# Optimization experiments

Hardware: AMD Instinct MI355X
Metric: run time of the kernel (lower is better)

Reference implementation:

```python
import jax, jax.numpy as jnp
import numpy as np

B, S, D, H, MLP = 2, 2048, 1024, 16, 4096
DH = D // H
EPS_LN = 1e-6
KERNEL_EPS = 1e-3  # fast_attention generalized kernel_epsilon


def layer_norm(x, scale, bias):
    m = jnp.mean(x, axis=-1, keepdims=True)
    v = jnp.mean(jnp.square(x - m), axis=-1, keepdims=True)
    return (x - m) * jax.lax.rsqrt(v + EPS_LN) * scale + bias


def performer_causal_attention(q, k, v):
    """FAVOR+ generalized attention (deterministic relu features), causal.

    q,k,v: [B,S,H,DH]. phi(x) = relu(x) + eps. Linear-time via prefix sums:
      out_i = phi(q_i) . cumsum_j<=i phi(k_j) v_j^T / (phi(q_i) . cumsum phi(k_j))
    """
    phi_q = jax.nn.relu(q) + KERNEL_EPS          # [B,S,H,M]
    phi_k = jax.nn.relu(k) + KERNEL_EPS          # [B,S,H,M]
    kv = jnp.cumsum(jnp.einsum('bshm,bshd->bshmd', phi_k, v), axis=1)  # [B,S,H,M,DH]
    num = jnp.einsum('bshm,bshmd->bshd', phi_q, kv)
    den = jnp.einsum('bshm,bshm->bsh', phi_q, jnp.cumsum(phi_k, axis=1))
    return num / den[..., None]


def setup_inputs() -> dict:
    key = jax.random.key(0)
    ks = jax.random.split(key, 7)
    def w(k, shape, scale):
        return jax.random.normal(k, shape, jnp.float32) * scale
    s_in = 1.0 / np.sqrt(D)
    return {
        'inputs': jax.random.normal(ks[0], (B, S, D), jnp.float32),
        'ln1_scale': jnp.ones((D,), jnp.float32),
        'ln1_bias': jnp.zeros((D,), jnp.float32),
        'wq': w(ks[1], (D, H, DH), s_in),
        'wk': w(ks[2], (D, H, DH), s_in),
        'wv': w(ks[3], (D, H, DH), s_in),
        'wo': w(ks[4], (H, DH, D), s_in),
        'ln2_scale': jnp.ones((D,), jnp.float32),
        'ln2_bias': jnp.zeros((D,), jnp.float32),
        'w1': w(ks[5], (D, MLP), s_in),
        'b1': jnp.zeros((MLP,), jnp.float32),
        'w2': w(ks[6], (MLP, D), 1.0 / np.sqrt(MLP)),
        'b2': jnp.zeros((D,), jnp.float32),
    }


def reference(inputs, ln1_scale, ln1_bias, wq, wk, wv, wo,
              ln2_scale, ln2_bias, w1, b1, w2, b2):
    # pre-LN self-attention (Performer FAVOR+ generalized, causal)
    x = layer_norm(inputs, ln1_scale, ln1_bias)
    q = jnp.einsum('bsd,dhm->bshm', x, wq)
    k = jnp.einsum('bsd,dhm->bshm', x, wk)
    v = jnp.einsum('bsd,dhm->bshm', x, wv)
    attn = performer_causal_attention(q, k, v)          # [B,S,H,DH]
    attn_out = jnp.einsum('bshm,hmd->bsd', attn, wo)    # output projection
    x = attn_out + inputs                               # residual
    # pre-LN MLP block
    y = layer_norm(x, ln2_scale, ln2_bias)
    y = jax.nn.gelu(y @ w1 + b1) @ w2 + b2
    return x + y
```

## Files before the change

### kernel.cpp

```cpp
#include <hip/hip_runtime.h>
#include <math.h>
#include <stdint.h>

typedef __bf16 bf16;
typedef bf16  bf16x8 __attribute__((ext_vector_type(8)));
typedef float f32x4  __attribute__((ext_vector_type(4)));

constexpr int Bb  = 2;
constexpr int Ss  = 2048;
constexpr int Dd  = 1024;
constexpr int Hh  = 16;
constexpr int DHh = 64;
constexpr int MLPd = 4096;
constexpr int ROWS = Bb * Ss;
constexpr int NC  = Ss / 64;
constexpr int BH  = Bb * Hh;
constexpr float EPS_LN = 1e-6f;
constexpr float KEPS   = 1e-3f;

__device__ __forceinline__ void async_copy16(const bf16* g, bf16* l) {
    __builtin_amdgcn_global_load_lds(
        (__attribute__((address_space(1))) void*)g,
        (__attribute__((address_space(3))) void*)l,
        16, 0, 0);
}

__device__ __forceinline__ int swz64(int row, int col) {
    return row * 64 + (((col >> 3) ^ row) & 7) * 8 + (col & 7);
}

__global__ __launch_bounds__(256) void ln_kernel(const float* __restrict__ x,
                                                 const float* __restrict__ scale,
                                                 const float* __restrict__ bias,
                                                 bf16* __restrict__ out)
{
    const int row = blockIdx.x;
    const float* xr = x + (size_t)row * Dd;
    float vals[4];
    float sum = 0.f, sumsq = 0.f;
#pragma unroll
    for (int i = 0; i < 4; i++) {
        float v = xr[threadIdx.x + 256 * i];
        vals[i] = v;
        sum += v;
        sumsq += v * v;
    }
#pragma unroll
    for (int off = 32; off > 0; off >>= 1) {
        sum   += __shfl_down(sum, off);
        sumsq += __shfl_down(sumsq, off);
    }
    __shared__ float ssum[4], ssq[4];
    const int wave = threadIdx.x >> 6;
    if ((threadIdx.x & 63) == 0) { ssum[wave] = sum; ssq[wave] = sumsq; }
    __syncthreads();
    const float tot   = ssum[0] + ssum[1] + ssum[2] + ssum[3];
    const float totsq = ssq[0] + ssq[1] + ssq[2] + ssq[3];
    const float mean = tot * (1.f / Dd);
    const float var  = totsq * (1.f / Dd) - mean * mean;
    const float r = rsqrtf(var + EPS_LN);
    bf16* orow = out + (size_t)row * Dd;
#pragma unroll
    for (int i = 0; i < 4; i++) {
        const int c = threadIdx.x + 256 * i;
        orow[c] = (bf16)((vals[i] - mean) * r * scale[c] + bias[c]);
    }
}

__global__ __launch_bounds__(256) void convert_T(const float* __restrict__ in,
                                                 bf16* __restrict__ out,
                                                 int K, int N)
{
    __shared__ float tile[32][33];
    const int k0 = blockIdx.y * 32, n0 = blockIdx.x * 32;
    const int tx = threadIdx.x & 31, ty = threadIdx.x >> 5;
#pragma unroll
    for (int i = 0; i < 32; i += 8)
        tile[ty + i][tx] = in[(size_t)(k0 + ty + i) * N + n0 + tx];
    __syncthreads();
#pragma unroll
    for (int i = 0; i < 32; i += 8)
        out[(size_t)(n0 + ty + i) * K + k0 + tx] = (bf16)tile[tx][ty + i];
}

__global__ __launch_bounds__(256) void convert_T4(const float* __restrict__ s0,
                                                  const float* __restrict__ s1,
                                                  const float* __restrict__ s2,
                                                  const float* __restrict__ s3,
                                                  bf16* __restrict__ d0,
                                                  bf16* __restrict__ d1,
                                                  bf16* __restrict__ d2,
                                                  bf16* __restrict__ d3)
{
    const float* in  = (blockIdx.z == 0) ? s0 : (blockIdx.z == 1) ? s1
                     : (blockIdx.z == 2) ? s2 : s3;
    bf16* out        = (blockIdx.z == 0) ? d0 : (blockIdx.z == 1) ? d1
                     : (blockIdx.z == 2) ? d2 : d3;
    __shared__ float tile[32][33];
    const int k0 = blockIdx.y * 32, n0 = blockIdx.x * 32;
    const int tx = threadIdx.x & 31, ty = threadIdx.x >> 5;
#pragma unroll
    for (int i = 0; i < 32; i += 8)
        tile[ty + i][tx] = in[(size_t)(k0 + ty + i) * 1024 + n0 + tx];
    __syncthreads();
#pragma unroll
    for (int i = 0; i < 32; i += 8)
        out[(size_t)(n0 + ty + i) * 1024 + k0 + tx] = (bf16)tile[tx][ty + i];
}

enum { EP_QKV = 0, EP_NONE = 1, EP_RES = 2, EP_GELU = 3, EP_BIAS_RES = 4 };

template <int TN, int BK, int NDIM, int KDIM, int MODE>
__global__ __launch_bounds__(256) void mfma_gemm(const bf16* __restrict__ A,
                                                 const bf16* __restrict__ BT,
                                                 void* __restrict__ Cout,
                                                 const float* __restrict__ bias,
                                                 const float* __restrict__ res,
                                                 bf16* __restrict__ out2,
                                                 bf16* __restrict__ out3)
{
    constexpr int WCT = TN / 2;
    constexpr int NJ  = TN / 32;
    constexpr int NS  = BK / 32;
    constexpr int CPR = BK / 8;
    constexpr int RPI = 2048 / BK;
    __shared__ bf16 As[128 * BK];
    __shared__ bf16 Bs[TN * BK];
    const int t = threadIdx.x;
    const int wave = t >> 6, lane = t & 63;
    const int row0 = blockIdx.y * 128, col0 = blockIdx.x * TN;
    const int wr = wave >> 1, wc = wave & 1;

    const int srow = t / CPR;
    const int gch  = (t % CPR) ^ (srow & 7);
    const int sdst = t * 8;

    const bf16* gA = A  + (size_t)(row0 + srow) * KDIM + gch * 8;
    const bf16* gB = BT + (size_t)(col0 + srow) * KDIM + gch * 8;

    const int m = lane & 15, quad = lane >> 4;
    const int mx7 = m & 7;

    f32x4 acc[4][NJ] = {};

    for (int k0 = 0; k0 < KDIM; k0 += BK) {
        __syncthreads();
#pragma unroll
        for (int i = 0; i < 128 / RPI; i++)
            async_copy16(gA + (size_t)i * RPI * KDIM, &As[i * 2048 + sdst]);
#pragma unroll
        for (int i = 0; i < TN / RPI; i++)
            async_copy16(gB + (size_t)i * RPI * KDIM, &Bs[i * 2048 + sdst]);
        __syncthreads();

#pragma unroll
        for (int s = 0; s < NS; s++) {
            const int pco = ((s * 4 + quad) ^ mx7) * 8;
            bf16x8 aF[4], bF[NJ];
#pragma unroll
            for (int i = 0; i < 4; i++)
                aF[i] = *(const bf16x8*)&As[(wr * 64 + i * 16 + m) * BK + pco];
#pragma unroll
            for (int j = 0; j < NJ; j++)
                bF[j] = *(const bf16x8*)&Bs[(wc * WCT + j * 16 + m) * BK + pco];
#pragma unroll
            for (int i = 0; i < 4; i++)
#pragma unroll
                for (int j = 0; j < NJ; j++)
                    acc[i][j] = __builtin_amdgcn_mfma_f32_16x16x32_bf16(
                        aF[i], bF[j], acc[i][j], 0, 0, 0);
        }
        gA += BK;
        gB += BK;
    }

    bf16* qkv_dst = nullptr;
    int col_base = col0;
    bool do_phi = false;
    if constexpr (MODE == EP_QKV) {
        const int third = col0 >> 10;
        qkv_dst = (third == 0) ? (bf16*)Cout : (third == 1) ? out2 : out3;
        col_base = col0 & 1023;
        do_phi = (third < 2);
    }

#pragma unroll
    for (int i = 0; i < 4; i++) {
#pragma unroll
        for (int j = 0; j < NJ; j++) {
#pragma unroll
            for (int r = 0; r < 4; r++) {
                const int row = row0 + wr * 64 + i * 16 + quad * 4 + r;
                const int col = col0 + wc * WCT + j * 16 + m;
                float val = acc[i][j][r];
                if constexpr (MODE == EP_QKV) {
                    const int lc = col_base + wc * WCT + j * 16 + m;
                    if (do_phi) val = fmaxf(val, 0.f) + KEPS;
                    qkv_dst[(size_t)row * 1024 + lc] = (bf16)val;
                } else if constexpr (MODE == EP_NONE) {
                    ((bf16*)Cout)[(size_t)row * NDIM + col] = (bf16)val;
                } else if constexpr (MODE == EP_RES) {
                    ((float*)Cout)[(size_t)row * NDIM + col] = val + res[(size_t)row * NDIM + col];
                } else if constexpr (MODE == EP_GELU) {
                    val += bias[col];
                    const float u = 0.7978845608028654f * (val + 0.044715f * val * val * val);
                    const float e = __expf(2.f * u);
                    val = val * (1.f - 1.f / (e + 1.f));
                    ((bf16*)Cout)[(size_t)row * NDIM + col] = (bf16)val;
                } else {
                    val += bias[col] + res[(size_t)row * NDIM + col];
                    ((float*)Cout)[(size_t)row * NDIM + col] = val;
                }
            }
        }
    }
}

__global__ __launch_bounds__(256) void chunk_kv_kernel(const bf16* __restrict__ phik,
                                                       const bf16* __restrict__ v,
                                                       bf16* __restrict__ kvs,
                                                       float* __restrict__ ksums)
{
    const int c = blockIdx.x, bh = blockIdx.y;
    const int b = bh >> 4, h = bh & 15;
    __shared__ bf16 Kt[64 * 64];
    __shared__ bf16 Vt[64 * 64];
    const int t = threadIdx.x;
    const int wave = t >> 6, lane = t & 63;
    const int m16 = lane & 15, quad = lane >> 4;
    const int wr = wave >> 1, wc = wave & 1;
    const int f = t & 63, s4 = t >> 6;

#pragma unroll
    for (int i = 0; i < 16; i++) {
        const int s = s4 + 4 * i;
        const size_t g = ((size_t)((b * Ss + c * 64 + s) * Hh + h)) * DHh + f;
        Kt[swz64(f, s)] = phik[g];
        Vt[swz64(f, s)] = v[g];
    }
    __syncthreads();

    f32x4 acc[2][2] = {};
#pragma unroll
    for (int ks = 0; ks < 2; ks++) {
        bf16x8 aF[2], bF[2];
#pragma unroll
        for (int i = 0; i < 2; i++)
            aF[i] = *(const bf16x8*)&Kt[swz64(wr * 32 + i * 16 + m16, ks * 32 + quad * 8)];
#pragma unroll
        for (int j = 0; j < 2; j++)
            bF[j] = *(const bf16x8*)&Vt[swz64(wc * 32 + j * 16 + m16, ks * 32 + quad * 8)];
#pragma unroll
        for (int i = 0; i < 2; i++)
#pragma unroll
            for (int j = 0; j < 2; j++)
                acc[i][j] = __builtin_amdgcn_mfma_f32_16x16x32_bf16(
                    aF[i], bF[j], acc[i][j], 0, 0, 0);
    }

    const size_t base = ((size_t)bh * NC + c) * 4096;
#pragma unroll
    for (int i = 0; i < 2; i++)
#pragma unroll
        for (int j = 0; j < 2; j++)
#pragma unroll
            for (int r = 0; r < 4; r++) {
                const int mrow = wr * 32 + i * 16 + quad * 4 + r;
                const int dcol = wc * 32 + j * 16 + m16;
                kvs[base + mrow * 64 + dcol] = (bf16)acc[i][j][r];
            }

    if (t < 64) {
        float s_ = 0.f;
#pragma unroll
        for (int p = 0; p < 8; p++) {
            bf16x8 k8 = *(const bf16x8*)&Kt[t * 64 + p * 8];
#pragma unroll
            for (int e = 0; e < 8; e++) s_ += (float)k8[e];
        }
        ksums[((size_t)bh * NC + c) * 64 + t] = s_;
    }
}

__global__ __launch_bounds__(256) void scan_kernel(bf16* __restrict__ kvs,
                                                   float* __restrict__ ksums)
{
    const int e  = blockIdx.x * 256 + threadIdx.x;
    const int bh = blockIdx.y;
    float run = 0.f;
#pragma unroll 4
    for (int c = 0; c < NC; c++) {
        const size_t idx = ((size_t)bh * NC + c) * 4096 + e;
        const float val = (float)kvs[idx];
        kvs[idx] = (bf16)run;
        run += val;
    }
    if (blockIdx.x == 0 && threadIdx.x < 64) {
        float r = 0.f;
        for (int c = 0; c < NC; c++) {
            const size_t idx = ((size_t)bh * NC + c) * 64 + threadIdx.x;
            const float val = ksums[idx];
            ksums[idx] = r;
            r += val;
        }
    }
}

__global__ __launch_bounds__(256) void attn_out_kernel(const bf16* __restrict__ phiq,
                                                       const bf16* __restrict__ phik,
                                                       const bf16* __restrict__ v,
                                                       const bf16* __restrict__ kvs,
                                                       const float* __restrict__ ksums,
                                                       bf16* __restrict__ attn)
{
    const int c = blockIdx.x, bh = blockIdx.y;
    const int b = bh >> 4, h = bh & 15;
    __shared__ bf16 Qs [64 * 64];
    __shared__ bf16 KVb[64 * 64];
    __shared__ bf16 Sm [64 * 64];
    __shared__ bf16 KVt[64 * 64];
    __shared__ float ksm[64], den[64];
    const int t = threadIdx.x;
    const int wave = t >> 6, lane = t & 63;
    const int m16 = lane & 15, quad = lane >> 4;
    const int wr = wave >> 1, wc = wave & 1;
    const int f = t & 63, s4 = t >> 6;

#pragma unroll
    for (int i = 0; i < 16; i++) {
        const int s = s4 + 4 * i;
        const size_t g = ((size_t)((b * Ss + c * 64 + s) * Hh + h)) * DHh + f;
        Qs [swz64(s, f)] = phiq[g];
        KVb[swz64(s, f)] = phik[g];
    }
    if (t < 64) ksm[t] = ksums[((size_t)bh * NC + c) * 64 + t];
    __syncthreads();

    f32x4 sacc[2][2] = {};
#pragma unroll
    for (int ks = 0; ks < 2; ks++) {
        bf16x8 aF[2], bF[2];
#pragma unroll
        for (int i = 0; i < 2; i++)
            aF[i] = *(const bf16x8*)&Qs [swz64(wr * 32 + i * 16 + m16, ks * 32 + quad * 8)];
#pragma unroll
        for (int j = 0; j < 2; j++)
            bF[j] = *(const bf16x8*)&KVb[swz64(wc * 32 + j * 16 + m16, ks * 32 + quad * 8)];
#pragma unroll
        for (int i = 0; i < 2; i++)
#pragma unroll
            for (int j = 0; j < 2; j++)
                sacc[i][j] = __builtin_amdgcn_mfma_f32_16x16x32_bf16(
                    aF[i], bF[j], sacc[i][j], 0, 0, 0);
    }
#pragma unroll
    for (int i = 0; i < 2; i++)
#pragma unroll
        for (int j = 0; j < 2; j++)
#pragma unroll
            for (int r = 0; r < 4; r++) {
                const int row = wr * 32 + i * 16 + quad * 4 + r;
                const int col = wc * 32 + j * 16 + m16;
                Sm[swz64(row, col)] = (bf16)((col <= row) ? sacc[i][j][r] : 0.f);
            }
    __syncthreads();

#pragma unroll
    for (int i = 0; i < 16; i++) {
        const int s = s4 + 4 * i;
        const size_t g = ((size_t)((b * Ss + c * 64 + s) * Hh + h)) * DHh + f;
        KVb[swz64(f, s)] = v[g];
    }
    {
        const size_t base = ((size_t)bh * NC + c) * 4096;
#pragma unroll
        for (int i = 0; i < 16; i++) {
            const int e = t + 256 * i;
            KVt[swz64(e & 63, e >> 6)] = kvs[base + e];
        }
    }
    __syncthreads();

    if (t < 64) {
        float d_ = 0.f;
#pragma unroll
        for (int p = 0; p < 8; p++) {
            const int gc = (p ^ (t & 7)) * 8;
            bf16x8 q8 = *(const bf16x8*)&Qs[t * 64 + p * 8];
            bf16x8 s8 = *(const bf16x8*)&Sm[t * 64 + p * 8];
#pragma unroll
            for (int e = 0; e < 8; e++)
                d_ += (float)q8[e] * ksm[gc + e] + (float)s8[e];
        }
        den[t] = d_;
    }

    f32x4 oacc[2][2] = {};
#pragma unroll
    for (int ks = 0; ks < 2; ks++) {
        bf16x8 aF[2], bF[2];
#pragma unroll
        for (int i = 0; i < 2; i++)
            aF[i] = *(const bf16x8*)&Sm [swz64(wr * 32 + i * 16 + m16, ks * 32 + quad * 8)];
#pragma unroll
        for (int j = 0; j < 2; j++)
            bF[j] = *(const bf16x8*)&KVb[swz64(wc * 32 + j * 16 + m16, ks * 32 + quad * 8)];
#pragma unroll
        for (int i = 0; i < 2; i++)
#pragma unroll
            for (int j = 0; j < 2; j++)
                oacc[i][j] = __builtin_amdgcn_mfma_f32_16x16x32_bf16(
                    aF[i], bF[j], oacc[i][j], 0, 0, 0);
    }
#pragma unroll
    for (int ks = 0; ks < 2; ks++) {
        bf16x8 aF[2], bF[2];
#pragma unroll
        for (int i = 0; i < 2; i++)
            aF[i] = *(const bf16x8*)&Qs [swz64(wr * 32 + i * 16 + m16, ks * 32 + quad * 8)];
#pragma unroll
        for (int j = 0; j < 2; j++)
            bF[j] = *(const bf16x8*)&KVt[swz64(wc * 32 + j * 16 + m16, ks * 32 + quad * 8)];
#pragma unroll
        for (int i = 0; i < 2; i++)
#pragma unroll
            for (int j = 0; j < 2; j++)
                oacc[i][j] = __builtin_amdgcn_mfma_f32_16x16x32_bf16(
                    aF[i], bF[j], oacc[i][j], 0, 0, 0);
    }
    __syncthreads();

#pragma unroll
    for (int i = 0; i < 2; i++) {
#pragma unroll
        for (int r = 0; r < 4; r++) {
            const int row = wr * 32 + i * 16 + quad * 4 + r;
            const float dinv = 1.f / den[row];
#pragma unroll
            for (int j = 0; j < 2; j++) {
                const int col = wc * 32 + j * 16 + m16;
                attn[((size_t)((b * Ss + c * 64 + row) * Hh + h)) * DHh + col] =
                    (bf16)(oacc[i][j][r] * dinv);
            }
        }
    }
}

extern "C" void kernel_launch(void* const* d_in, const int* in_sizes, int n_in,
                              void* d_out, int out_size, void* d_ws, size_t ws_size,
                              hipStream_t stream)
{
    const float* inputs    = (const float*)d_in[0];
    const float* ln1_scale = (const float*)d_in[1];
    const float* ln1_bias  = (const float*)d_in[2];
    const float* wq        = (const float*)d_in[3];
    const float* wk        = (const float*)d_in[4];
    const float* wv        = (const float*)d_in[5];
    const float* wo        = (const float*)d_in[6];
    const float* ln2_scale = (const float*)d_in[7];
    const float* ln2_bias  = (const float*)d_in[8];
    const float* w1        = (const float*)d_in[9];
    const float* b1        = (const float*)d_in[10];
    const float* w2        = (const float*)d_in[11];
    const float* b2        = (const float*)d_in[12];
    float* out = (float*)d_out;

    char* ws = (char*)d_ws;
    bf16*  xln   = (bf16*)ws;
    bf16*  q     = (bf16*)(ws + (8ull  << 20));
    bf16*  k     = (bf16*)(ws + (16ull << 20));
    bf16*  v     = (bf16*)(ws + (24ull << 20));
    bf16*  kvs   = (bf16*)(ws + (32ull << 20));
    float* x2    = (float*)(ws + (48ull << 20));
    float* ksums = (float*)(ws + (64ull << 20));
    bf16*  wqT   = (bf16*)(ws + (64ull << 20) + (1ull << 18));
    bf16*  wkT   = wqT + 1024 * 1024;
    bf16*  wvT   = wkT + 1024 * 1024;
    bf16*  woT   = wvT + 1024 * 1024;
    bf16*  w1T   = woT + 1024 * 1024;
    bf16*  w2T   = w1T + 4096 * 1024;
    bf16*  attn  = xln;
    bf16*  yln   = q;
    bf16*  hbuf  = k;

    convert_T4<<<dim3(32, 32, 4), 256, 0, stream>>>(wq, wk, wv, wo, wqT, wkT, wvT, woT);
    convert_T<<<dim3(4096 / 32, 1024 / 32), 256, 0, stream>>>(w1, w1T, 1024, 4096);
    convert_T<<<dim3(1024 / 32, 4096 / 32), 256, 0, stream>>>(w2, w2T, 4096, 1024);

    ln_kernel<<<ROWS, 256, 0, stream>>>(inputs, ln1_scale, ln1_bias, xln);

    mfma_gemm<128, 64, 3072, 1024, EP_QKV><<<dim3(3072 / 128, ROWS / 128), 256, 0, stream>>>(
        xln, wqT, q, nullptr, nullptr, k, v);

    {
        dim3 gridA(NC, BH);
        chunk_kv_kernel<<<gridA, 256, 0, stream>>>(k, v, kvs, ksums);
        scan_kernel<<<dim3(4096 / 256, BH), 256, 0, stream>>>(kvs, ksums);
        attn_out_kernel<<<gridA, 256, 0, stream>>>(q, k, v, kvs, ksums, attn);
    }

    mfma_gemm<64, 128, 1024, 1024, EP_RES><<<dim3(1024 / 64, ROWS / 128), 256, 0, stream>>>(
        attn, woT, x2, nullptr, inputs, nullptr, nullptr);

    ln_kernel<<<ROWS, 256, 0, stream>>>(x2, ln2_scale, ln2_bias, yln);

    mfma_gemm<128, 64, 4096, 1024, EP_GELU><<<dim3(MLPd / 128, ROWS / 128), 256, 0, stream>>>(
        yln, w1T, hbuf, b1, nullptr, nullptr, nullptr);
    mfma_gemm<64, 128, 1024, 4096, EP_BIAS_RES><<<dim3(1024 / 64, ROWS / 128), 256, 0, stream>>>(
        hbuf, w2T, out, b2, x2, nullptr, nullptr);
}
```

Baseline: 313.3 us.

## Store residual stream in bf16, remap GEMM blocks per XCD, contiguous LN loads

The intermediate residual x2 is now stored as bf16 instead of fp32. This halves the write traffic in the Wo GEMM epilogue and the reads in LN2 and the final residual add. GEMM grids become 1D, and block IDs are remapped so each XCD (block id mod 8) owns a contiguous band of 128-row tiles, aiming for better L2 reuse of A rows. LN kernels now read four contiguous elements per thread. Rounding the residual stream to bf16 lowers accuracy and risks tolerance failures.

```diff
diff --git a/kernel.cpp b/kernel.cpp
--- a/kernel.cpp
+++ b/kernel.cpp
@@ -29,18 +29,20 @@
     return row * 64 + (((col >> 3) ^ row) & 7) * 8 + (col & 7);
 }
 
-__global__ __launch_bounds__(256) void ln_kernel(const float* __restrict__ x,
+template <typename T>
+__global__ __launch_bounds__(256) void ln_kernel(const T* __restrict__ x,
                                                  const float* __restrict__ scale,
                                                  const float* __restrict__ bias,
                                                  bf16* __restrict__ out)
 {
     const int row = blockIdx.x;
-    const float* xr = x + (size_t)row * Dd;
+    const T* xr = x + (size_t)row * Dd;
+    const int c0 = threadIdx.x * 4;
     float vals[4];
     float sum = 0.f, sumsq = 0.f;
 #pragma unroll
     for (int i = 0; i < 4; i++) {
-        float v = xr[threadIdx.x + 256 * i];
+        float v = (float)xr[c0 + i];
         vals[i] = v;
         sum += v;
         sumsq += v * v;
@@ -61,10 +63,8 @@
     const float r = rsqrtf(var + EPS_LN);
     bf16* orow = out + (size_t)row * Dd;
 #pragma unroll
-    for (int i = 0; i < 4; i++) {
-        const int c = threadIdx.x + 256 * i;
-        orow[c] = (bf16)((vals[i] - mean) * r * scale[c] + bias[c]);
-    }
+    for (int i = 0; i < 4; i++)
+        orow[c0 + i] = (bf16)((vals[i] - mean) * r * scale[c0 + i] + bias[c0 + i]);
 }
 
 __global__ __launch_bounds__(256) void convert_T(const float* __restrict__ in,
@@ -115,7 +115,7 @@
                                                  const bf16* __restrict__ BT,
                                                  void* __restrict__ Cout,
                                                  const float* __restrict__ bias,
-                                                 const float* __restrict__ res,
+                                                 const void* __restrict__ res,
                                                  bf16* __restrict__ out2,
                                                  bf16* __restrict__ out3)
 {
@@ -124,11 +124,18 @@
     constexpr int NS  = BK / 32;
     constexpr int CPR = BK / 8;
     constexpr int RPI = 2048 / BK;
+    constexpr int GRIDY = 32;
+    constexpr int RPX = GRIDY / 8;
     __shared__ bf16 As[128 * BK];
     __shared__ bf16 Bs[TN * BK];
     const int t = threadIdx.x;
     const int wave = t >> 6, lane = t & 63;
-    const int row0 = blockIdx.y * 128, col0 = blockIdx.x * TN;
+
+    const int bid = blockIdx.x;
+    const int xcd = bid & 7, idx = bid >> 3;
+    const int row0 = (xcd * RPX + (idx & (RPX - 1))) * 128;
+    const int col0 = (idx / RPX) * TN;
+
     const int wr = wave >> 1, wc = wave & 1;
 
     const int srow = t / CPR;
@@ -200,7 +207,8 @@
                 } else if constexpr (MODE == EP_NONE) {
                     ((bf16*)Cout)[(size_t)row * NDIM + col] = (bf16)val;
                 } else if constexpr (MODE == EP_RES) {
-                    ((float*)Cout)[(size_t)row * NDIM + col] = val + res[(size_t)row * NDIM + col];
+                    val += ((const float*)res)[(size_t)row * NDIM + col];
+                    ((bf16*)Cout)[(size_t)row * NDIM + col] = (bf16)val;
                 } else if constexpr (MODE == EP_GELU) {
                     val += bias[col];
                     const float u = 0.7978845608028654f * (val + 0.044715f * val * val * val);
@@ -208,7 +216,7 @@
                     val = val * (1.f - 1.f / (e + 1.f));
                     ((bf16*)Cout)[(size_t)row * NDIM + col] = (bf16)val;
                 } else {
-                    val += bias[col] + res[(size_t)row * NDIM + col];
+                    val += bias[col] + (float)((const bf16*)res)[(size_t)row * NDIM + col];
                     ((float*)Cout)[(size_t)row * NDIM + col] = val;
                 }
             }
@@ -471,7 +479,7 @@
     bf16*  k     = (bf16*)(ws + (16ull << 20));
     bf16*  v     = (bf16*)(ws + (24ull << 20));
     bf16*  kvs   = (bf16*)(ws + (32ull << 20));
-    float* x2    = (float*)(ws + (48ull << 20));
+    bf16*  x2    = (bf16*)(ws + (48ull << 20));
     float* ksums = (float*)(ws + (64ull << 20));
     bf16*  wqT   = (bf16*)(ws + (64ull << 20) + (1ull << 18));
     bf16*  wkT   = wqT + 1024 * 1024;
@@ -487,9 +495,9 @@
     convert_T<<<dim3(4096 / 32, 1024 / 32), 256, 0, stream>>>(w1, w1T, 1024, 4096);
     convert_T<<<dim3(1024 / 32, 4096 / 32), 256, 0, stream>>>(w2, w2T, 4096, 1024);
 
-    ln_kernel<<<ROWS, 256, 0, stream>>>(inputs, ln1_scale, ln1_bias, xln);
-
-    mfma_gemm<128, 64, 3072, 1024, EP_QKV><<<dim3(3072 / 128, ROWS / 128), 256, 0, stream>>>(
+    ln_kernel<float><<<ROWS, 256, 0, stream>>>(inputs, ln1_scale, ln1_bias, xln);
+
+    mfma_gemm<128, 64, 3072, 1024, EP_QKV><<<dim3(24 * 32), 256, 0, stream>>>(
         xln, wqT, q, nullptr, nullptr, k, v);
 
     {
@@ -499,13 +507,13 @@
         attn_out_kernel<<<gridA, 256, 0, stream>>>(q, k, v, kvs, ksums, attn);
     }
 
-    mfma_gemm<64, 128, 1024, 1024, EP_RES><<<dim3(1024 / 64, ROWS / 128), 256, 0, stream>>>(
+    mfma_gemm<64, 128, 1024, 1024, EP_RES><<<dim3(16 * 32), 256, 0, stream>>>(
         attn, woT, x2, nullptr, inputs, nullptr, nullptr);
 
-    ln_kernel<<<ROWS, 256, 0, stream>>>(x2, ln2_scale, ln2_bias, yln);
-
-    mfma_gemm<128, 64, 4096, 1024, EP_GELU><<<dim3(MLPd / 128, ROWS / 128), 256, 0, stream>>>(
+    ln_kernel<bf16><<<ROWS, 256, 0, stream>>>(x2, ln2_scale, ln2_bias, yln);
+
+    mfma_gemm<128, 64, 4096, 1024, EP_GELU><<<dim3(32 * 32), 256, 0, stream>>>(
         yln, w1T, hbuf, b1, nullptr, nullptr, nullptr);
-    mfma_gemm<64, 128, 1024, 4096, EP_BIAS_RES><<<dim3(1024 / 64, ROWS / 128), 256, 0, stream>>>(
+    mfma_gemm<64, 128, 1024, 4096, EP_BIAS_RES><<<dim3(16 * 32), 256, 0, stream>>>(
         hbuf, w2T, out, b2, x2, nullptr, nullptr);
 }
```

Result: faster. 304.5 us (-2.8%).
